# Performance work log

Measured on AMD Instinct MI355X. Metric: run time of the kernel, lower is better.

Reference implementation:

```python
import jax, jax.numpy as jnp
import numpy as np

T, A, E, RAW, H, NACT, NTP = 64, 48, 22, 512, 256, 21, 3
# entity_distinct: self entity [0], friendly entities [1:12], hostile entities [12:22]
PARAM_SHAPES = [
    ("W1", (NTP, RAW, H)), ("b1", (NTP, H)), ("W2", (NTP, H, H)), ("b2", (NTP, H)),
    ("WCf", (NTP, 2 * H, H)), ("bCf", (NTP, H)), ("WMf", (NTP, 2 * H + 2 * RAW, H)), ("bMf", (NTP, H)),
    ("WCh", (NTP, 2 * H, H)), ("bCh", (NTP, H)), ("WMh", (NTP, 2 * H + 2 * RAW, H)), ("bMh", (NTP, H)),
    ("L1", (NTP, 2 * H, H)), ("bL1", (NTP, H)), ("L2", (NTP, H, H // 2)), ("bL2", (NTP, H // 2)),
    ("L3", (NTP, H // 2, NACT)), ("bL3", (NTP, NACT)),
    ("V1", (NTP, 2 * H, H)), ("bV1", (NTP, H)), ("V2", (NTP, H, 1)), ("bV2", (NTP, 1)),
]
PNAMES = [n for n, _ in PARAM_SHAPES]


def setup_inputs() -> dict:
    key = jax.random.key(0)
    ks = jax.random.split(key, 3 + len(PARAM_SHAPES))
    inp = {
        "obs": jax.random.normal(ks[0], (T, A, E, RAW), jnp.float32),
        "hete_pick": jax.random.randint(ks[1], (T, A), 0, NTP, jnp.int32),
        "dead": jax.random.bernoulli(ks[2], 0.15, (T, A, E)),
    }
    for i, (n, s) in enumerate(PARAM_SHAPES):
        inp[n] = jax.random.normal(ks[3 + i], s, jnp.float32) * 0.02
    return inp


def _net_forward(p, obs, dead):
    relu = jax.nn.relu
    obs = jnp.where(dead[..., None], 0.0, obs)                    # nan_to_num for dead entities
    v = relu(obs @ p["W1"] + p["b1"]) @ p["W2"] + p["b2"]         # [T,A,E,H] per-entity encoder
    zs, ze_f, ze_h = obs[..., 0, :], obs[..., 1:12, :], obs[..., 12:22, :]
    vs, ve_f, ve_h = v[..., 0, :], v[..., 1:12, :], v[..., 12:22, :]
    df, dh = dead[..., 1:12], dead[..., 12:22]

    def conc(ve, d, ze, WC, bC, WM, bM):
        w = (~d).astype(obs.dtype)                                # alive mask [T,A,Ef]
        denom = jnp.maximum(w.sum(-1, keepdims=True), 1.0)
        pool = jnp.einsum('taeh,tae->tah', ve, w) / denom         # masked mean over entities
        pool_z = jnp.einsum('taer,tae->tar', ze, w) / denom       # skip-connect raw-obs pool
        vC = relu(jnp.concatenate([vs, pool], -1) @ WC + bC)
        vM = relu(jnp.concatenate([vs, pool, zs, pool_z], -1) @ WM + bM)
        return vC, vM

    vfC, vfM = conc(ve_f, df, ze_f, p["WCf"], p["bCf"], p["WMf"], p["bMf"])
    vhC, vhM = conc(ve_h, dh, ze_h, p["WCh"], p["bCh"], p["WMh"], p["bMh"])
    vC = jnp.concatenate([vfC, vhC], -1)                          # [T,A,2H] dual-conc fuse
    vM = jnp.concatenate([vfM, vhM], -1)
    logits = relu(relu(vC @ p["L1"] + p["bL1"]) @ p["L2"] + p["bL2"]) @ p["L3"] + p["bL3"]
    value = relu(vM @ p["V1"] + p["bV1"]) @ p["V2"] + p["bV2"]    # [T,A,1]
    logp = jax.nn.log_softmax(logits, -1)
    act = jnp.argmax(logits, -1)                                  # deterministic (test_mode) action
    alp = jnp.take_along_axis(logp, act[..., None], -1)           # [T,A,1] action log-prob
    return act, value, alp


def reference(obs, hete_pick, dead, W1, b1, W2, b2, WCf, bCf, WMf, bMf, WCh, bCh, WMh, bMh,
              L1, bL1, L2, bL2, L3, bL3, V1, bV1, V2, bV2):
    params = dict(W1=W1, b1=b1, W2=W2, b2=b2, WCf=WCf, bCf=bCf, WMf=WMf, bMf=bMf,
                  WCh=WCh, bCh=bCh, WMh=WMh, bMh=bMh, L1=L1, bL1=bL1, L2=L2, bL2=bL2,
                  L3=L3, bL3=bL3, V1=V1, bV1=bV1, V2=V2, bV2=bV2)
    act = jnp.zeros((T, A), jnp.int32)
    value = jnp.zeros((T, A, 1), obs.dtype)
    alp = jnp.zeros((T, A, 1), obs.dtype)
    for t in range(NTP):                                          # heterogeneous dispatch (distribute_compute)
        pt = {k: v[t] for k, v in params.items()}
        a_t, v_t, lp_t = _net_forward(pt, obs, dead)
        m = hete_pick == t                                        # mask_arr[t]
        act = jnp.where(m, a_t.astype(jnp.int32), act)
        value = jnp.where(m[..., None], v_t, value)
        alp = jnp.where(m[..., None], lp_t, alp)
    return act, value, alp
```

## Files before the change

### kernel.cpp

```cpp
#include <hip/hip_runtime.h>
#include <cstdint>

#define T_ 64
#define A_ 48
#define NP_ 3072
#define E_ 22
#define RAW_ 512
#define H_ 256
#define NACT_ 21
#define NTP_ 3
#define PV_ 3456
#define RV_ 68096
#define NDEAD_ 67584

typedef unsigned short u16;
typedef __attribute__((ext_vector_type(8))) short short8;
typedef __attribute__((ext_vector_type(4))) short short4v;
typedef __attribute__((ext_vector_type(4))) float floatx4;

__device__ __forceinline__ u16 f2bf(float x) {
    unsigned u = __float_as_uint(x);
    unsigned r = (u + 0x7FFFu + ((u >> 16) & 1u)) >> 16;
    return (u16)r;
}
__device__ __forceinline__ float bf2f(u16 h) {
    return __uint_as_float(((unsigned)h) << 16);
}

__global__ void k_bucket(const unsigned* __restrict__ deadRaw,
                         const int* __restrict__ hete, int* __restrict__ wsI)
{
    __shared__ int fl[2];
    __shared__ int sc[3], cur[3], sps[3], srs[3];
    int tid = threadIdx.x;
    if (tid < 2) fl[tid] = 0;
    if (tid < 3) { sc[tid] = 0; cur[tid] = 0; }
    __syncthreads();
    int ni = 0, nf = 0;
    for (int i = tid; i < 1024; i += 256) {
        unsigned w = deadRaw[i];
        if (w > 1u) ni = 1;
        if (w != 0u && w != 0x3F800000u) nf = 1;
    }
    if (ni) atomicOr(&fl[0], 1);
    if (nf) atomicOr(&fl[1], 1);
    for (int p = tid; p < NP_; p += 256) atomicAdd(&sc[hete[p]], 1);
    __syncthreads();
    if (tid == 0) {
        int c0 = sc[0], c1 = sc[1], c2 = sc[2];
        int p1 = (c0 + 127) & ~127;
        int p2 = p1 + ((c1 + 127) & ~127);
        sps[0] = 0; sps[1] = p1; sps[2] = p2;
        int r1 = (22 * c0 + 127) & ~127;
        int r2 = r1 + ((22 * c1 + 127) & ~127);
        srs[0] = 0; srs[1] = r1; srs[2] = r2;
        wsI[0] = fl[0] ? (fl[1] ? 2 : 1) : 0;
        wsI[1] = c0; wsI[2] = c1; wsI[3] = c2;
        wsI[4] = 0; wsI[5] = p1; wsI[6] = p2;
        wsI[8] = 0; wsI[9] = r1; wsI[10] = r2;
    }
    __syncthreads();
    int* pairIdx = wsI + 16;
    int* prb = pairIdx + PV_;
    for (int pv = tid; pv < PV_; pv += 256) pairIdx[pv] = -1;
    __syncthreads();
    for (int p = tid; p < NP_; p += 256) {
        int t = hete[p];
        int pos = atomicAdd(&cur[t], 1);
        pairIdx[sps[t] + pos] = p;
    }
    for (int pv = tid; pv < PV_; pv += 256) {
        int t = (pv >= sps[1]) + (pv >= sps[2]);
        prb[pv] = srs[t] + 22 * (pv - sps[t]);
    }
}

__global__ void k_deadmask(const void* __restrict__ dead,
                           const int* __restrict__ wsI, float* __restrict__ dm)
{
    int i = blockIdx.x * 256 + threadIdx.x;
    if (i >= NDEAD_) return;
    int mode = wsI[0];
    bool d;
    if (mode == 0)      d = ((const int*)dead)[i] != 0;
    else if (mode == 1) d = ((const float*)dead)[i] != 0.f;
    else                d = ((const unsigned char*)dead)[i] != 0;
    dm[i] = d ? 0.f : 1.f;
}

__global__ void k_rowobs(const int* __restrict__ cnt, const int* __restrict__ ps,
                         const int* __restrict__ rs, const int* __restrict__ pairIdx,
                         const float* __restrict__ dm, int* __restrict__ rowObs)
{
    int rv = blockIdx.x * 256 + threadIdx.x;
    if (rv >= RV_) return;
    int t = (rv >= rs[1]) + (rv >= rs[2]);
    int local = rv - rs[t];
    int out = -1;
    if (local < 22 * cnt[t]) {
        int pl = local / 22;
        int e = local - pl * 22;
        int p = pairIdx[ps[t] + pl];
        if (p >= 0) {
            int oi = p * 22 + e;
            if (dm[oi] != 0.f) out = oi;
        }
    }
    rowObs[rv] = out;
}

__global__ void k_wconv(const float* __restrict__ W, u16* __restrict__ Hi,
                        u16* __restrict__ Lo, int K)
{
    int K8 = K >> 3;
    int kc = blockIdx.x % K8;
    int t  = blockIdx.x / K8;
    int n  = threadIdx.x;
    const float* w = W + (long)t * K * 256 + n;
    short8 hv, lv;
#pragma unroll
    for (int j = 0; j < 8; ++j) {
        float x = w[(long)(kc * 8 + j) * 256];
        u16 hh = f2bf(x);
        hv[j] = (short)hh;
        lv[j] = (short)f2bf(x - bf2f(hh));
    }
    long o = ((long)t * 256 + n) * K + kc * 8;
    *(short8*)(Hi + o) = hv;
    *(short8*)(Lo + o) = lv;
}

#define AST 40
template<bool GATHER, bool RELU>
__global__ __launch_bounds__(256) void k_mgemm(
    const float* __restrict__ A0, const float* __restrict__ A1, int lda,
    const int* __restrict__ rowIdx,
    const u16* __restrict__ Bh0, const u16* __restrict__ Bl0,
    const u16* __restrict__ Bh1, const u16* __restrict__ Bl1,
    const float* __restrict__ bias0, const float* __restrict__ bias1,
    float* __restrict__ C0, float* __restrict__ C1, int ldc,
    int coff0, int coff1,
    const int* __restrict__ starts, int K)
{
    __shared__ short Ah[128 * AST], Al[128 * AST];
    __shared__ short Bh[128 * AST], Bl[128 * AST];

    const int tid = threadIdx.x;
    const int z = blockIdx.z;
    const float* A = z ? A1 : A0;
    const u16* Bhi = z ? Bh1 : Bh0;
    const u16* Blo = z ? Bl1 : Bl0;
    const float* bias = z ? bias1 : bias0;
    float* C = z ? C1 : C0;
    const int coff = z ? coff1 : coff0;

    const long rb = (long)blockIdx.x * 128;
    const int n0 = blockIdx.y * 128;
    const int t = (rb >= starts[0]) + (rb >= starts[1]);
    const u16* bhp = Bhi + ((long)t * 256 + n0) * K;
    const u16* blp = Blo + ((long)t * 256 + n0) * K;
    const float* biasT = bias + (long)t * 256 + n0;

    const int ar = tid >> 3;
    const int ac = (tid & 7) * 4;
    long arow[4]; float amask[4];
#pragma unroll
    for (int it = 0; it < 4; ++it) {
        int r = 32 * it + ar;
        if (GATHER) {
            int i0 = rowIdx[rb + r];
            amask[it] = (i0 < 0) ? 0.f : 1.f;
            arow[it] = (i0 < 0) ? 0 : (long)i0 * lda;
        } else {
            amask[it] = 1.f;
            arow[it] = (rb + r) * (long)lda;
        }
    }
    const int bn = tid >> 2;
    const int bc = (tid & 3) * 8;

    const int wave = tid >> 6;
    const int lane = tid & 63;
    const int wr = (wave >> 1) * 64;
    const int wc = (wave & 1) * 64;
    const int lm = lane & 15;
    const int quad = lane >> 4;

    floatx4 acc[4][4];
#pragma unroll
    for (int i = 0; i < 4; ++i)
#pragma unroll
        for (int j = 0; j < 4; ++j) acc[i][j] = (floatx4){0.f, 0.f, 0.f, 0.f};

    for (int k0 = 0; k0 < K; k0 += 32) {
        float4 av[4];
#pragma unroll
        for (int it = 0; it < 4; ++it)
            av[it] = *(const float4*)(A + arow[it] + k0 + ac);
        short8 bhv[2], blv[2];
#pragma unroll
        for (int it = 0; it < 2; ++it) {
            long off = (long)(64 * it + bn) * K + k0 + bc;
            bhv[it] = *(const short8*)(bhp + off);
            blv[it] = *(const short8*)(blp + off);
        }
        __syncthreads();
#pragma unroll
        for (int it = 0; it < 4; ++it) {
            float xs[4] = {av[it].x, av[it].y, av[it].z, av[it].w};
            short4v hv, lv;
#pragma unroll
            for (int e = 0; e < 4; ++e) {
                float x = GATHER ? xs[e] * amask[it] : xs[e];
                u16 hh = f2bf(x);
                hv[e] = (short)hh;
                lv[e] = (short)f2bf(x - bf2f(hh));
            }
            int r = 32 * it + ar;
            *(short4v*)&Ah[r * AST + ac] = hv;
            *(short4v*)&Al[r * AST + ac] = lv;
        }
#pragma unroll
        for (int it = 0; it < 2; ++it) {
            int n = 64 * it + bn;
            *(short8*)&Bh[n * AST + bc] = bhv[it];
            *(short8*)&Bl[n * AST + bc] = blv[it];
        }
        __syncthreads();
        short8 fah[4], fal[4];
#pragma unroll
        for (int i = 0; i < 4; ++i) {
            int m = wr + 16 * i + lm;
            fah[i] = *(const short8*)&Ah[m * AST + quad * 8];
            fal[i] = *(const short8*)&Al[m * AST + quad * 8];
        }
#pragma unroll
        for (int j = 0; j < 4; ++j) {
            int n = wc + 16 * j + lm;
            short8 fbh = *(const short8*)&Bh[n * AST + quad * 8];
            short8 fbl = *(const short8*)&Bl[n * AST + quad * 8];
#pragma unroll
            for (int i = 0; i < 4; ++i) {
                acc[i][j] = __builtin_amdgcn_mfma_f32_16x16x32_bf16(fah[i], fbh, acc[i][j], 0, 0, 0);
                acc[i][j] = __builtin_amdgcn_mfma_f32_16x16x32_bf16(fal[i], fbh, acc[i][j], 0, 0, 0);
                acc[i][j] = __builtin_amdgcn_mfma_f32_16x16x32_bf16(fah[i], fbl, acc[i][j], 0, 0, 0);
            }
        }
    }
#pragma unroll
    for (int j = 0; j < 4; ++j) {
        int col = wc + 16 * j + lm;
        float bj = biasT[col];
#pragma unroll
        for (int i = 0; i < 4; ++i) {
            long rbase = rb + wr + 16 * i + quad * 4;
#pragma unroll
            for (int r = 0; r < 4; ++r) {
                float vv = acc[i][j][r] + bj;
                if (RELU) vv = fmaxf(vv, 0.f);
                C[(rbase + r) * (long)ldc + coff + n0 + col] = vv;
            }
        }
    }
}

__global__ __launch_bounds__(256) void k_prep(
    const int* __restrict__ pairIdx, const int* __restrict__ prb,
    const float* __restrict__ dm, const float* __restrict__ v,
    const float* __restrict__ obs,
    float* __restrict__ XF, float* __restrict__ XH)
{
    int pv = blockIdx.x, c = threadIdx.x;
    int p = pairIdx[pv];
    float* xf = XF + (long)pv * 1536;
    float* xh = XH + (long)pv * 1536;
    if (p < 0) {
        for (int s = 0; s < 6; ++s) { xf[s * 256 + c] = 0.f; xh[s * 256 + c] = 0.f; }
        return;
    }
    __shared__ float sw[22];
    if (c < 22) sw[c] = dm[p * 22 + c];
    __syncthreads();
    float denf = 0.f, denh = 0.f;
    for (int e = 1; e < 12; ++e)  denf += sw[e];
    for (int e = 12; e < 22; ++e) denh += sw[e];
    denf = 1.f / fmaxf(denf, 1.f);
    denh = 1.f / fmaxf(denh, 1.f);

    long base = prb[pv];
    float vs = v[base * 256 + c];
    xf[c] = vs; xh[c] = vs;
    float af = 0.f, ah = 0.f;
    for (int e = 1; e < 12; ++e)  af += sw[e] * v[(base + e) * 256 + c];
    for (int e = 12; e < 22; ++e) ah += sw[e] * v[(base + e) * 256 + c];
    xf[256 + c] = af * denf;
    xh[256 + c] = ah * denh;
    const float* ob = obs + (long)p * 22 * 512;
    float w0 = sw[0];
    float z0 = ob[c] * w0;
    float z1 = ob[256 + c] * w0;
    xf[512 + c] = z0; xh[512 + c] = z0;
    xf[768 + c] = z1; xh[768 + c] = z1;
#pragma unroll
    for (int half = 0; half < 2; ++half) {
        int c2 = c + half * 256;
        float zf = 0.f, zh = 0.f;
        for (int e = 1; e < 12; ++e)  zf += sw[e] * ob[(long)e * 512 + c2];
        for (int e = 12; e < 22; ++e) zh += sw[e] * ob[(long)e * 512 + c2];
        xf[1024 + c2] = zf * denf;
        xh[1024 + c2] = zh * denh;
    }
}

__global__ __launch_bounds__(128) void k_final(
    const float* __restrict__ g1, const float* __restrict__ vV,
    const float* __restrict__ L2, const float* __restrict__ bL2,
    const float* __restrict__ L3, const float* __restrict__ bL3,
    const float* __restrict__ V2, const float* __restrict__ bV2,
    const int* __restrict__ pairIdx, const int* __restrict__ ps,
    float* __restrict__ out)
{
    int pv = blockIdx.x;
    int p = pairIdx[pv];
    if (p < 0) return;
    int c = threadIdx.x;
    int t = (pv >= ps[1]) + (pv >= ps[2]);

    __shared__ float sg1[256], sg2[128], sval[2];
    const float* g1p = g1 + (long)pv * 256;
    sg1[c] = g1p[c];
    sg1[c + 128] = g1p[c + 128];

    const float* vv = vV + (long)pv * 256;
    const float* v2t = V2 + t * 256;
    float s = vv[c] * v2t[c] + vv[c + 128] * v2t[c + 128];
    for (int off = 32; off; off >>= 1) s += __shfl_down(s, off);
    if ((c & 63) == 0) sval[c >> 6] = s;
    __syncthreads();

    const float* l2 = L2 + (long)t * 256 * 128 + c;
    float a = bL2[t * 128 + c];
#pragma unroll 8
    for (int k = 0; k < 256; ++k) a = fmaf(sg1[k], l2[(long)k * 128], a);
    sg2[c] = fmaxf(a, 0.f);
    __syncthreads();

    if (c < 64) {
        float lg = -3.0e38f;
        if (c < 21) {
            const float* l3t = L3 + (long)t * 128 * 21 + c;
            float acc = bL3[t * 21 + c];
            for (int k = 0; k < 128; ++k) acc = fmaf(sg2[k], l3t[k * 21], acc);
            lg = acc;
        }
        float mv = lg; int mi = (c < 21) ? c : 9999;
        for (int off = 32; off; off >>= 1) {
            float ov = __shfl_down(mv, off);
            int oi = __shfl_down(mi, off);
            if (ov > mv || (ov == mv && oi < mi)) { mv = ov; mi = oi; }
        }
        mv = __shfl(mv, 0); mi = __shfl(mi, 0);
        float e = (c < 21) ? expf(lg - mv) : 0.f;
        for (int off = 32; off; off >>= 1) e += __shfl_down(e, off);
        if (c == 0) {
            out[p] = (float)mi;
            out[NP_ + p] = sval[0] + sval[1] + bV2[t];
            out[2 * NP_ + p] = -logf(e);
        }
    }
}

extern "C" void kernel_launch(void* const* d_in, const int* in_sizes, int n_in,
                              void* d_out, int out_size, void* d_ws, size_t ws_size,
                              hipStream_t stream)
{
    const float* obs = (const float*)d_in[0];
    const int* hete = (const int*)d_in[1];
    const void* dead = d_in[2];
    const float* W1 = (const float*)d_in[3];  const float* b1 = (const float*)d_in[4];
    const float* W2 = (const float*)d_in[5];  const float* b2 = (const float*)d_in[6];
    const float* WCf = (const float*)d_in[7]; const float* bCf = (const float*)d_in[8];
    const float* WMf = (const float*)d_in[9]; const float* bMf = (const float*)d_in[10];
    const float* WCh = (const float*)d_in[11]; const float* bCh = (const float*)d_in[12];
    const float* WMh = (const float*)d_in[13]; const float* bMh = (const float*)d_in[14];
    const float* L1 = (const float*)d_in[15]; const float* bL1 = (const float*)d_in[16];
    const float* L2 = (const float*)d_in[17]; const float* bL2 = (const float*)d_in[18];
    const float* L3 = (const float*)d_in[19]; const float* bL3 = (const float*)d_in[20];
    const float* V1 = (const float*)d_in[21]; const float* bV1 = (const float*)d_in[22];
    const float* V2 = (const float*)d_in[23]; const float* bV2 = (const float*)d_in[24];
    float* out = (float*)d_out;

    int* wsI = (int*)d_ws;
    int* pairIdx = wsI + 16;
    int* prb = pairIdx + PV_;
    int* rowObs = prb + PV_;
    long fbase = ((16L + PV_ + PV_ + RV_) + 63) & ~63L;
    float* wsF = (float*)d_ws;
    float* dm = wsF + fbase;
    float* cur = dm + NDEAD_;
    auto allocUS = [&](long K) { u16* p = (u16*)cur; cur += (3L * 256 * K) / 2; return p; };
    u16* W1h = allocUS(512);  u16* W1l = allocUS(512);
    u16* W2h = allocUS(256);  u16* W2l = allocUS(256);
    u16* WCfh = allocUS(512); u16* WCfl = allocUS(512);
    u16* WChh = allocUS(512); u16* WChl = allocUS(512);
    u16* WMfh = allocUS(1536); u16* WMfl = allocUS(1536);
    u16* WMhh = allocUS(1536); u16* WMhl = allocUS(1536);
    u16* L1h = allocUS(512);  u16* L1l = allocUS(512);
    u16* V1h = allocUS(512);  u16* V1l = allocUS(512);
    float* regA = cur;
    float* regB = regA + (long)RV_ * 256;
    float* h1 = regA;
    float* XF = regA;
    float* XH = XF + (long)PV_ * 1536;
    float* v = regB;
    float* vC = regB;
    float* vM = vC + (long)PV_ * 512;
    float* g1 = vM + (long)PV_ * 512;
    float* vV = g1 + (long)PV_ * 256;

    k_bucket<<<1, 256, 0, stream>>>((const unsigned*)dead, hete, wsI);
    k_deadmask<<<264, 256, 0, stream>>>(dead, wsI, dm);
    k_rowobs<<<266, 256, 0, stream>>>(wsI + 1, wsI + 4, wsI + 8, pairIdx, dm, rowObs);

    k_wconv<<<3 * 512 / 8, 256, 0, stream>>>(W1, W1h, W1l, 512);
    k_wconv<<<3 * 256 / 8, 256, 0, stream>>>(W2, W2h, W2l, 256);
    k_wconv<<<3 * 512 / 8, 256, 0, stream>>>(WCf, WCfh, WCfl, 512);
    k_wconv<<<3 * 512 / 8, 256, 0, stream>>>(WCh, WChh, WChl, 512);
    k_wconv<<<3 * 1536 / 8, 256, 0, stream>>>(WMf, WMfh, WMfl, 1536);
    k_wconv<<<3 * 1536 / 8, 256, 0, stream>>>(WMh, WMhh, WMhl, 1536);
    k_wconv<<<3 * 512 / 8, 256, 0, stream>>>(L1, L1h, L1l, 512);
    k_wconv<<<3 * 512 / 8, 256, 0, stream>>>(V1, V1h, V1l, 512);

    k_mgemm<true, true><<<dim3(RV_ / 128, 2, 1), 256, 0, stream>>>(
        obs, obs, 512, rowObs, W1h, W1l, W1h, W1l, b1, b1,
        h1, h1, 256, 0, 0, wsI + 9, 512);
    k_mgemm<false, false><<<dim3(RV_ / 128, 2, 1), 256, 0, stream>>>(
        h1, h1, 256, nullptr, W2h, W2l, W2h, W2l, b2, b2,
        v, v, 256, 0, 0, wsI + 9, 256);

    k_prep<<<PV_, 256, 0, stream>>>(pairIdx, prb, dm, v, obs, XF, XH);

    k_mgemm<false, true><<<dim3(PV_ / 128, 2, 2), 256, 0, stream>>>(
        XF, XH, 1536, nullptr, WCfh, WCfl, WChh, WChl, bCf, bCh,
        vC, vC, 512, 0, 256, wsI + 5, 512);
    k_mgemm<false, true><<<dim3(PV_ / 128, 2, 2), 256, 0, stream>>>(
        XF, XH, 1536, nullptr, WMfh, WMfl, WMhh, WMhl, bMf, bMh,
        vM, vM, 512, 0, 256, wsI + 5, 1536);
    k_mgemm<false, true><<<dim3(PV_ / 128, 2, 2), 256, 0, stream>>>(
        vC, vM, 512, nullptr, L1h, L1l, V1h, V1l, bL1, bV1,
        g1, vV, 256, 0, 0, wsI + 5, 512);

    k_final<<<PV_, 128, 0, stream>>>(g1, vV, L2, bL2, L3, bL3, V2, bV2,
                                     pairIdx, wsI + 4, out);
    (void)in_sizes; (void)n_in; (void)out_size; (void)ws_size;
}
```

Before: 617.6 us.

## Store GEMM intermediates as split bf16 and load tiles via direct global-to-LDS

Intermediate activations (h1, XF/XH, vC/vM) are now written as hi/lo bf16 pairs by the producing kernels, so the consuming GEMMs can copy A and B tiles straight into LDS with global_load_lds. The padded LDS layout is replaced by an XOR swizzle to limit bank conflicts. Several smaller changes ride along: the eight weight-conversion launches become one batched launch, the WC and WM GEMMs are merged into a single 4-way z launch, and bf16 rounding uses the hardware v_cvt_pk_bf16_f32 instruction. The swizzle adds index arithmetic, and the direct loads drop the separate register staging step, which may expose load latency.

After: 565.2 us. -8.5%, faster.

```diff
diff --git a/kernel.cpp b/kernel.cpp
--- a/kernel.cpp
+++ b/kernel.cpp
@@ -19,12 +19,18 @@
 typedef __attribute__((ext_vector_type(4))) float floatx4;
 
 __device__ __forceinline__ u16 f2bf(float x) {
-    unsigned u = __float_as_uint(x);
-    unsigned r = (u + 0x7FFFu + ((u >> 16) & 1u)) >> 16;
+    unsigned r;
+    asm("v_cvt_pk_bf16_f32 %0, %1, %1" : "=v"(r) : "v"(x));
     return (u16)r;
 }
 __device__ __forceinline__ float bf2f(u16 h) {
     return __uint_as_float(((unsigned)h) << 16);
+}
+
+typedef __attribute__((address_space(1))) const void* gp_t;
+typedef __attribute__((address_space(3))) void* lp_t;
+__device__ __forceinline__ void gload16(const void* g, void* l) {
+    __builtin_amdgcn_global_load_lds((gp_t)g, (lp_t)l, 16, 0, 0);
 }
 
 __global__ void k_bucket(const unsigned* __restrict__ deadRaw,
@@ -109,14 +115,22 @@
     rowObs[rv] = out;
 }
 
-__global__ void k_wconv(const float* __restrict__ W, u16* __restrict__ Hi,
-                        u16* __restrict__ Lo, int K)
-{
+struct WCA {
+    const float* W[8]; u16* Hi[8]; u16* Lo[8]; int K[8]; int bs[9];
+};
+__global__ __launch_bounds__(256) void k_wconv(WCA a)
+{
+    int blk = blockIdx.x;
+    int s = 0;
+#pragma unroll
+    for (int i = 1; i < 8; ++i) if (blk >= a.bs[i]) s = i;
+    int lb = blk - a.bs[s];
+    int K = a.K[s];
     int K8 = K >> 3;
-    int kc = blockIdx.x % K8;
-    int t  = blockIdx.x / K8;
+    int kc = lb % K8;
+    int t  = lb / K8;
     int n  = threadIdx.x;
-    const float* w = W + (long)t * K * 256 + n;
+    const float* w = a.W[s] + (long)t * K * 256 + n;
     short8 hv, lv;
 #pragma unroll
     for (int j = 0; j < 8; ++j) {
@@ -126,58 +140,53 @@
         lv[j] = (short)f2bf(x - bf2f(hh));
     }
     long o = ((long)t * 256 + n) * K + kc * 8;
-    *(short8*)(Hi + o) = hv;
-    *(short8*)(Lo + o) = lv;
-}
-
-#define AST 40
-template<bool GATHER, bool RELU>
+    *(short8*)(a.Hi[s] + o) = hv;
+    *(short8*)(a.Lo[s] + o) = lv;
+}
+
+struct GD {
+    const void* Aa; const void* Ab;
+    const u16* Bh; const u16* Bl;
+    const float* bias;
+    void* Ca; void* Cb;
+    long lda; long ldc;
+    int K; int coff;
+};
+struct GA4 { GD d[4]; };
+
+template<int AMODE, bool RELU, int OUTS>
 __global__ __launch_bounds__(256) void k_mgemm(
-    const float* __restrict__ A0, const float* __restrict__ A1, int lda,
-    const int* __restrict__ rowIdx,
-    const u16* __restrict__ Bh0, const u16* __restrict__ Bl0,
-    const u16* __restrict__ Bh1, const u16* __restrict__ Bl1,
-    const float* __restrict__ bias0, const float* __restrict__ bias1,
-    float* __restrict__ C0, float* __restrict__ C1, int ldc,
-    int coff0, int coff1,
-    const int* __restrict__ starts, int K)
-{
-    __shared__ short Ah[128 * AST], Al[128 * AST];
-    __shared__ short Bh[128 * AST], Bl[128 * AST];
-
+    GA4 ga, const int* __restrict__ rowIdx, const int* __restrict__ starts)
+{
+    __shared__ short Ah[128 * 32], Al[128 * 32], Bh[128 * 32], Bl[128 * 32];
     const int tid = threadIdx.x;
-    const int z = blockIdx.z;
-    const float* A = z ? A1 : A0;
-    const u16* Bhi = z ? Bh1 : Bh0;
-    const u16* Blo = z ? Bl1 : Bl0;
-    const float* bias = z ? bias1 : bias0;
-    float* C = z ? C1 : C0;
-    const int coff = z ? coff1 : coff0;
-
+    const GD d = ga.d[blockIdx.z];
     const long rb = (long)blockIdx.x * 128;
     const int n0 = blockIdx.y * 128;
     const int t = (rb >= starts[0]) + (rb >= starts[1]);
-    const u16* bhp = Bhi + ((long)t * 256 + n0) * K;
-    const u16* blp = Blo + ((long)t * 256 + n0) * K;
-    const float* biasT = bias + (long)t * 256 + n0;
+    const int K = d.K;
+    const long lda = d.lda;
+    const u16* bhT = d.Bh + ((long)t * 256 + n0) * K;
+    const u16* blT = d.Bl + ((long)t * 256 + n0) * K;
+    const float* biasT = d.bias + (long)t * 256 + n0;
+
+    const int cs = tid & 3;
 
     const int ar = tid >> 3;
     const int ac = (tid & 7) * 4;
     long arow[4]; float amask[4];
-#pragma unroll
-    for (int it = 0; it < 4; ++it) {
-        int r = 32 * it + ar;
-        if (GATHER) {
+    const float* Afp = (const float*)d.Aa;
+    if (AMODE == 1) {
+#pragma unroll
+        for (int it = 0; it < 4; ++it) {
+            int r = 32 * it + ar;
             int i0 = rowIdx[rb + r];
             amask[it] = (i0 < 0) ? 0.f : 1.f;
             arow[it] = (i0 < 0) ? 0 : (long)i0 * lda;
-        } else {
-            amask[it] = 1.f;
-            arow[it] = (rb + r) * (long)lda;
-        }
-    }
-    const int bn = tid >> 2;
-    const int bc = (tid & 3) * 8;
+        }
+    }
+    const u16* ahT = (const u16*)d.Aa;
+    const u16* alT = (const u16*)d.Ab;
 
     const int wave = tid >> 6;
     const int lane = tid & 63;
@@ -194,51 +203,62 @@
 
     for (int k0 = 0; k0 < K; k0 += 32) {
         float4 av[4];
-#pragma unroll
-        for (int it = 0; it < 4; ++it)
-            av[it] = *(const float4*)(A + arow[it] + k0 + ac);
-        short8 bhv[2], blv[2];
-#pragma unroll
-        for (int it = 0; it < 2; ++it) {
-            long off = (long)(64 * it + bn) * K + k0 + bc;
-            bhv[it] = *(const short8*)(bhp + off);
-            blv[it] = *(const short8*)(blp + off);
+        if (AMODE == 1) {
+#pragma unroll
+            for (int it = 0; it < 4; ++it)
+                av[it] = *(const float4*)(Afp + arow[it] + k0 + ac);
         }
         __syncthreads();
 #pragma unroll
-        for (int it = 0; it < 4; ++it) {
-            float xs[4] = {av[it].x, av[it].y, av[it].z, av[it].w};
-            short4v hv, lv;
-#pragma unroll
-            for (int e = 0; e < 4; ++e) {
-                float x = GATHER ? xs[e] * amask[it] : xs[e];
-                u16 hh = f2bf(x);
-                hv[e] = (short)hh;
-                lv[e] = (short)f2bf(x - bf2f(hh));
+        for (int i = 0; i < 2; ++i) {
+            int c = i * 256 + tid;
+            int r = c >> 2;
+            long go = (long)r * K + k0 + ((cs ^ (r & 3)) << 3);
+            gload16(bhT + go, &Bh[c << 3]);
+            gload16(blT + go, &Bl[c << 3]);
+        }
+        if (AMODE == 0) {
+#pragma unroll
+            for (int i = 0; i < 2; ++i) {
+                int c = i * 256 + tid;
+                int r = c >> 2;
+                long go = (rb + r) * lda + k0 + ((cs ^ (r & 3)) << 3);
+                gload16(ahT + go, &Ah[c << 3]);
+                gload16(alT + go, &Al[c << 3]);
             }
-            int r = 32 * it + ar;
-            *(short4v*)&Ah[r * AST + ac] = hv;
-            *(short4v*)&Al[r * AST + ac] = lv;
-        }
-#pragma unroll
-        for (int it = 0; it < 2; ++it) {
-            int n = 64 * it + bn;
-            *(short8*)&Bh[n * AST + bc] = bhv[it];
-            *(short8*)&Bl[n * AST + bc] = blv[it];
+        } else {
+#pragma unroll
+            for (int it = 0; it < 4; ++it) {
+                float xs[4] = {av[it].x, av[it].y, av[it].z, av[it].w};
+                short4v hv, lv;
+#pragma unroll
+                for (int e = 0; e < 4; ++e) {
+                    float x = xs[e] * amask[it];
+                    u16 hh = f2bf(x);
+                    hv[e] = (short)hh;
+                    lv[e] = (short)f2bf(x - bf2f(hh));
+                }
+                int r = 32 * it + ar;
+                int bs = ((((ac >> 3) ^ (r & 3))) << 4) | ((ac & 4) << 1);
+                *(short4v*)((char*)Ah + r * 64 + bs) = hv;
+                *(short4v*)((char*)Al + r * 64 + bs) = lv;
+            }
         }
         __syncthreads();
         short8 fah[4], fal[4];
 #pragma unroll
         for (int i = 0; i < 4; ++i) {
             int m = wr + 16 * i + lm;
-            fah[i] = *(const short8*)&Ah[m * AST + quad * 8];
-            fal[i] = *(const short8*)&Al[m * AST + quad * 8];
+            int sl = (quad ^ (m & 3)) << 3;
+            fah[i] = *(const short8*)&Ah[(m << 5) + sl];
+            fal[i] = *(const short8*)&Al[(m << 5) + sl];
         }
 #pragma unroll
         for (int j = 0; j < 4; ++j) {
             int n = wc + 16 * j + lm;
-            short8 fbh = *(const short8*)&Bh[n * AST + quad * 8];
-            short8 fbl = *(const short8*)&Bl[n * AST + quad * 8];
+            int sl = (quad ^ (n & 3)) << 3;
+            short8 fbh = *(const short8*)&Bh[(n << 5) + sl];
+            short8 fbl = *(const short8*)&Bl[(n << 5) + sl];
 #pragma unroll
             for (int i = 0; i < 4; ++i) {
                 acc[i][j] = __builtin_amdgcn_mfma_f32_16x16x32_bf16(fah[i], fbh, acc[i][j], 0, 0, 0);
@@ -258,7 +278,14 @@
             for (int r = 0; r < 4; ++r) {
                 float vv = acc[i][j][r] + bj;
                 if (RELU) vv = fmaxf(vv, 0.f);
-                C[(rbase + r) * (long)ldc + coff + n0 + col] = vv;
+                long off = (rbase + r) * d.ldc + d.coff + n0 + col;
+                if (OUTS == 0) {
+                    ((float*)d.Ca)[off] = vv;
+                } else {
+                    u16 hh = f2bf(vv);
+                    ((u16*)d.Ca)[off] = hh;
+                    ((u16*)d.Cb)[off] = f2bf(vv - bf2f(hh));
+                }
             }
         }
     }
@@ -268,14 +295,17 @@
     const int* __restrict__ pairIdx, const int* __restrict__ prb,
     const float* __restrict__ dm, const float* __restrict__ v,
     const float* __restrict__ obs,
-    float* __restrict__ XF, float* __restrict__ XH)
+    u16* __restrict__ XFh, u16* __restrict__ XFl,
+    u16* __restrict__ XHh, u16* __restrict__ XHl)
 {
     int pv = blockIdx.x, c = threadIdx.x;
     int p = pairIdx[pv];
-    float* xf = XF + (long)pv * 1536;
-    float* xh = XH + (long)pv * 1536;
+    long xo = (long)pv * 1536;
     if (p < 0) {
-        for (int s = 0; s < 6; ++s) { xf[s * 256 + c] = 0.f; xh[s * 256 + c] = 0.f; }
+        for (int s = 0; s < 6; ++s) {
+            XFh[xo + s * 256 + c] = 0; XFl[xo + s * 256 + c] = 0;
+            XHh[xo + s * 256 + c] = 0; XHl[xo + s * 256 + c] = 0;
+        }
         return;
     }
     __shared__ float sw[22];
@@ -287,28 +317,35 @@
     denf = 1.f / fmaxf(denf, 1.f);
     denh = 1.f / fmaxf(denh, 1.f);
 
+    auto wsp = [&](u16* Hh, u16* Hl, long idx, float val) {
+        u16 hh = f2bf(val);
+        Hh[idx] = hh;
+        Hl[idx] = f2bf(val - bf2f(hh));
+    };
+
     long base = prb[pv];
     float vs = v[base * 256 + c];
-    xf[c] = vs; xh[c] = vs;
+    wsp(XFh, XFl, xo + c, vs);
+    wsp(XHh, XHl, xo + c, vs);
     float af = 0.f, ah = 0.f;
     for (int e = 1; e < 12; ++e)  af += sw[e] * v[(base + e) * 256 + c];
     for (int e = 12; e < 22; ++e) ah += sw[e] * v[(base + e) * 256 + c];
-    xf[256 + c] = af * denf;
-    xh[256 + c] = ah * denh;
+    wsp(XFh, XFl, xo + 256 + c, af * denf);
+    wsp(XHh, XHl, xo + 256 + c, ah * denh);
     const float* ob = obs + (long)p * 22 * 512;
     float w0 = sw[0];
     float z0 = ob[c] * w0;
     float z1 = ob[256 + c] * w0;
-    xf[512 + c] = z0; xh[512 + c] = z0;
-    xf[768 + c] = z1; xh[768 + c] = z1;
+    wsp(XFh, XFl, xo + 512 + c, z0); wsp(XHh, XHl, xo + 512 + c, z0);
+    wsp(XFh, XFl, xo + 768 + c, z1); wsp(XHh, XHl, xo + 768 + c, z1);
 #pragma unroll
     for (int half = 0; half < 2; ++half) {
         int c2 = c + half * 256;
         float zf = 0.f, zh = 0.f;
         for (int e = 1; e < 12; ++e)  zf += sw[e] * ob[(long)e * 512 + c2];
         for (int e = 12; e < 22; ++e) zh += sw[e] * ob[(long)e * 512 + c2];
-        xf[1024 + c2] = zf * denf;
-        xh[1024 + c2] = zh * denh;
+        wsp(XFh, XFl, xo + 1024 + c2, zf * denf);
+        wsp(XHh, XHl, xo + 1024 + c2, zh * denh);
     }
 }
 
@@ -409,46 +446,66 @@
     u16* V1h = allocUS(512);  u16* V1l = allocUS(512);
     float* regA = cur;
     float* regB = regA + (long)RV_ * 256;
-    float* h1 = regA;
-    float* XF = regA;
-    float* XH = XF + (long)PV_ * 1536;
+
+    u16* h1h = (u16*)regA;
+    u16* h1l = h1h + (long)RV_ * 256;
+    u16* XFh = (u16*)regA;
+    u16* XFl = XFh + (long)PV_ * 1536;
+    u16* XHh = XFl + (long)PV_ * 1536;
+    u16* XHl = XHh + (long)PV_ * 1536;
     float* v = regB;
-    float* vC = regB;
-    float* vM = vC + (long)PV_ * 512;
-    float* g1 = vM + (long)PV_ * 512;
+    u16* vCh = (u16*)regB;
+    u16* vCl = vCh + (long)PV_ * 512;
+    u16* vMh = vCl + (long)PV_ * 512;
+    u16* vMl = vMh + (long)PV_ * 512;
+    float* g1 = (float*)(vMl + (long)PV_ * 512);
     float* vV = g1 + (long)PV_ * 256;
 
     k_bucket<<<1, 256, 0, stream>>>((const unsigned*)dead, hete, wsI);
     k_deadmask<<<264, 256, 0, stream>>>(dead, wsI, dm);
     k_rowobs<<<266, 256, 0, stream>>>(wsI + 1, wsI + 4, wsI + 8, pairIdx, dm, rowObs);
 
-    k_wconv<<<3 * 512 / 8, 256, 0, stream>>>(W1, W1h, W1l, 512);
-    k_wconv<<<3 * 256 / 8, 256, 0, stream>>>(W2, W2h, W2l, 256);
-    k_wconv<<<3 * 512 / 8, 256, 0, stream>>>(WCf, WCfh, WCfl, 512);
-    k_wconv<<<3 * 512 / 8, 256, 0, stream>>>(WCh, WChh, WChl, 512);
-    k_wconv<<<3 * 1536 / 8, 256, 0, stream>>>(WMf, WMfh, WMfl, 1536);
-    k_wconv<<<3 * 1536 / 8, 256, 0, stream>>>(WMh, WMhh, WMhl, 1536);
-    k_wconv<<<3 * 512 / 8, 256, 0, stream>>>(L1, L1h, L1l, 512);
-    k_wconv<<<3 * 512 / 8, 256, 0, stream>>>(V1, V1h, V1l, 512);
-
-    k_mgemm<true, true><<<dim3(RV_ / 128, 2, 1), 256, 0, stream>>>(
-        obs, obs, 512, rowObs, W1h, W1l, W1h, W1l, b1, b1,
-        h1, h1, 256, 0, 0, wsI + 9, 512);
-    k_mgemm<false, false><<<dim3(RV_ / 128, 2, 1), 256, 0, stream>>>(
-        h1, h1, 256, nullptr, W2h, W2l, W2h, W2l, b2, b2,
-        v, v, 256, 0, 0, wsI + 9, 256);
-
-    k_prep<<<PV_, 256, 0, stream>>>(pairIdx, prb, dm, v, obs, XF, XH);
-
-    k_mgemm<false, true><<<dim3(PV_ / 128, 2, 2), 256, 0, stream>>>(
-        XF, XH, 1536, nullptr, WCfh, WCfl, WChh, WChl, bCf, bCh,
-        vC, vC, 512, 0, 256, wsI + 5, 512);
-    k_mgemm<false, true><<<dim3(PV_ / 128, 2, 2), 256, 0, stream>>>(
-        XF, XH, 1536, nullptr, WMfh, WMfl, WMhh, WMhl, bMf, bMh,
-        vM, vM, 512, 0, 256, wsI + 5, 1536);
-    k_mgemm<false, true><<<dim3(PV_ / 128, 2, 2), 256, 0, stream>>>(
-        vC, vM, 512, nullptr, L1h, L1l, V1h, V1l, bL1, bV1,
-        g1, vV, 256, 0, 0, wsI + 5, 512);
+    {
+        WCA wa;
+        const float* Ws[8] = {W1, W2, WCf, WCh, WMf, WMh, L1, V1};
+        u16* His[8] = {W1h, W2h, WCfh, WChh, WMfh, WMhh, L1h, V1h};
+        u16* Los[8] = {W1l, W2l, WCfl, WChl, WMfl, WMhl, L1l, V1l};
+        int Ks[8] = {512, 256, 512, 512, 1536, 1536, 512, 512};
+        int acc_b = 0; wa.bs[0] = 0;
+        for (int i = 0; i < 8; ++i) {
+            wa.W[i] = Ws[i]; wa.Hi[i] = His[i]; wa.Lo[i] = Los[i]; wa.K[i] = Ks[i];
+            acc_b += 3 * Ks[i] / 8; wa.bs[i + 1] = acc_b;
+        }
+        k_wconv<<<acc_b, 256, 0, stream>>>(wa);
+    }
+
+    GA4 g;
+    auto setd = [&](int i, const void* Aa, const void* Ab, const u16* Bh_, const u16* Bl_,
+                    const float* bias, void* Ca, void* Cb, long lda_, long ldc_, int K_, int coff_) {
+        g.d[i] = GD{Aa, Ab, Bh_, Bl_, bias, Ca, Cb, lda_, ldc_, K_, coff_};
+    };
+
+    for (int i = 0; i < 4; ++i)
+        setd(i, obs, nullptr, W1h, W1l, b1, h1h, h1l, 512, 256, 512, 0);
+    k_mgemm<1, true, 1><<<dim3(RV_ / 128, 2, 1), 256, 0, stream>>>(g, rowObs, wsI + 9);
+
+    for (int i = 0; i < 4; ++i)
+        setd(i, h1h, h1l, W2h, W2l, b2, v, nullptr, 256, 256, 256, 0);
+    k_mgemm<0, false, 0><<<dim3(RV_ / 128, 2, 1), 256, 0, stream>>>(g, nullptr, wsI + 9);
+
+    k_prep<<<PV_, 256, 0, stream>>>(pairIdx, prb, dm, v, obs, XFh, XFl, XHh, XHl);
+
+    setd(0, XFh, XFl, WCfh, WCfl, bCf, vCh, vCl, 1536, 512, 512, 0);
+    setd(1, XHh, XHl, WChh, WChl, bCh, vCh, vCl, 1536, 512, 512, 256);
+    setd(2, XFh, XFl, WMfh, WMfl, bMf, vMh, vMl, 1536, 512, 1536, 0);
+    setd(3, XHh, XHl, WMhh, WMhl, bMh, vMh, vMl, 1536, 512, 1536, 256);
+    k_mgemm<0, true, 1><<<dim3(PV_ / 128, 2, 4), 256, 0, stream>>>(g, nullptr, wsI + 5);
+
+    setd(0, vCh, vCl, L1h, L1l, bL1, g1, nullptr, 512, 256, 512, 0);
+    setd(1, vMh, vMl, V1h, V1l, bV1, vV, nullptr, 512, 256, 512, 0);
+    setd(2, vCh, vCl, L1h, L1l, bL1, g1, nullptr, 512, 256, 512, 0);
+    setd(3, vCh, vCl, L1h, L1l, bL1, g1, nullptr, 512, 256, 512, 0);
+    k_mgemm<0, true, 0><<<dim3(PV_ / 128, 2, 2), 256, 0, stream>>>(g, nullptr, wsI + 5);
 
     k_final<<<PV_, 128, 0, stream>>>(g1, vV, L2, bL2, L3, bL3, V2, bV2,
                                      pairIdx, wsI + 4, out);
```
